# Optimization experiments

Measured on AMD Instinct MI355X. Metric: run time of the kernel, lower is better.

## Reference

```python
import jax, jax.numpy as jnp
import numpy as np

B, H, T, D = 4, 8, 1024, 64
DECAY = 0.95


def setup_inputs() -> dict:
    key = jax.random.key(0)
    kq, kk, kv = jax.random.split(key, 3)
    q = jax.random.normal(kq, (B, H, T, D), dtype=jnp.float32)
    k = jax.random.normal(kk, (B, H, T, D), dtype=jnp.float32)
    v = jax.random.normal(kv, (B, H, T, D), dtype=jnp.float32)
    return {"q": q, "k": k, "v": v}


def reference(q, k, v):
    """Recurrent KV (linear-attention) scan.

    State: S_t = decay * S_{t-1} + k_t outer v_t  (per batch/head, [D, D])
    Out:   o_t = q_t @ S_t                         ([D])
    """
    decay = jnp.float32(DECAY)

    def step(S, qkv_t):
        q_t, k_t, v_t = qkv_t  # each [B, H, D]
        S = decay * S + jnp.einsum('bhd,bhe->bhde', k_t, v_t)  # [B,H,D,D]
        o_t = jnp.einsum('bhd,bhde->bhe', q_t, S)              # [B,H,D]
        return S, o_t

    S0 = jnp.zeros((B, H, D, D), dtype=q.dtype)
    # time-major for scan: [T, B, H, D]
    qT = jnp.moveaxis(q, 2, 0)
    kT = jnp.moveaxis(k, 2, 0)
    vT = jnp.moveaxis(v, 2, 0)
    _, oT = jax.lax.scan(step, S0, (qT, kT, vT))
    return jnp.moveaxis(oT, 0, 2)  # [B, H, T, D]
```

## Files before the change

kernel.cpp:

```cpp
#include <hip/hip_runtime.h>
#include <hip/hip_bf16.h>

#define D_    64
#define BH    32
#define LCH   64
#define NC    16
#define DECAY 0.95f
#define LN_D  0.051293294f
#define DEC64 0.03752432f
#define LDSB  68

typedef __attribute__((ext_vector_type(8))) short          bf8_t;
typedef __attribute__((ext_vector_type(8))) unsigned short u16x8;
typedef __attribute__((ext_vector_type(4))) float          f32x4;
typedef unsigned short u16;

static __device__ __forceinline__ u16 f2bf(float f) {
    return __builtin_bit_cast(u16, __float2bfloat16(f));
}
static __device__ __forceinline__ bf8_t frag_rr(float4 a, float4 b, float sc) {
    u16x8 r;
    r[0] = f2bf(a.x * sc); r[1] = f2bf(a.y * sc); r[2] = f2bf(a.z * sc); r[3] = f2bf(a.w * sc);
    r[4] = f2bf(b.x * sc); r[5] = f2bf(b.y * sc); r[6] = f2bf(b.z * sc); r[7] = f2bf(b.w * sc);
    return __builtin_bit_cast(bf8_t, r);
}
static __device__ __forceinline__ bf8_t frag_g(const float* g) {
    u16x8 r;
    #pragma unroll
    for (int z = 0; z < 8; ++z) r[z] = f2bf(g[z]);
    return __builtin_bit_cast(bf8_t, r);
}

__global__ __launch_bounds__(256, 3) void kv_fused(const float* __restrict__ q,
                                                   const float* __restrict__ k,
                                                   const float* __restrict__ v,
                                                   float* __restrict__ o) {
    __shared__ u16 KT[2][D_][LDSB];
    __shared__ u16 VT[D_][LDSB];
    __shared__ u16 ST[D_][LDSB];
    __shared__ u16 As[LCH][LDSB];

    const int bid = (int)blockIdx.x;
    const int lb  = (bid & 7) * ((BH * NC) / 8) + (bid >> 3);
    const int bh  = lb >> 4;
    const int c   = lb & (NC - 1);

    const int tid  = threadIdx.x;
    const size_t bhb  = (size_t)bh * (NC * LCH) * D_;
    const size_t base = bhb + (size_t)c * LCH * D_;

    const int lane = tid & 63, w = tid >> 6;
    const int fr   = lane & 15, hi = lane >> 4;
    const int fk   = hi << 3;
    const int i0   = w << 4;
    const int ib   = i0 + (hi << 2);

    const int sj   = tid >> 2;
    const int sc0  = (tid & 3) << 4;
    const int sjx  = sj ^ ((tid & 3) << 4);

    float pv1[2][8], pv0[2][8];
    if (c >= 1) {
        const float* vs = v + base - (size_t)LCH * D_ + i0 + fr;
        #pragma unroll
        for (int kt = 0; kt < 2; ++kt)
            #pragma unroll
            for (int z = 0; z < 8; ++z)
                pv1[kt][z] = vs[(size_t)(kt * 32 + fk + z) * D_];
    }
    if (c >= 2) {
        const float* vs = v + base - (size_t)(2 * LCH) * D_ + i0 + fr;
        #pragma unroll
        for (int kt = 0; kt < 2; ++kt)
            #pragma unroll
            for (int z = 0; z < 8; ++z)
                pv0[kt][z] = vs[(size_t)(kt * 32 + fk + z) * D_];
    }
    const float* qrow = q + base + (size_t)(i0 + fr) * D_;
    const float4 qa0 = *(const float4*)(qrow + fk);
    const float4 qa1 = *(const float4*)(qrow + fk + 4);
    const float4 qb0 = *(const float4*)(qrow + 32 + fk);
    const float4 qb1 = *(const float4*)(qrow + 32 + fk + 4);
    float4 k1[4], k0[4];
    if (c >= 1) {
        const float* kg = k + base - (size_t)LCH * D_ + sj * D_ + sc0;
        #pragma unroll
        for (int m = 0; m < 4; ++m) k1[m] = *(const float4*)(kg + 4 * m);
    }
    if (c >= 2) {
        const float* kg = k + base - (size_t)(2 * LCH) * D_ + sj * D_ + sc0;
        #pragma unroll
        for (int m = 0; m < 4; ++m) k0[m] = *(const float4*)(kg + 4 * m);
    }
    float4 vo[4];
    {
        const float* vg = v + base + sj * D_ + sc0;
        #pragma unroll
        for (int m = 0; m < 4; ++m) vo[m] = *(const float4*)(vg + 4 * m);
    }

    const bf8_t aq0 = frag_rr(qa0, qa1, 1.f);
    const bf8_t aq1 = frag_rr(qb0, qb1, 1.f);
    bf8_t av1[2], av0[2];
    if (c >= 1) { av1[0] = frag_g(pv1[0]); av1[1] = frag_g(pv1[1]); }
    if (c >= 2) { av0[0] = frag_g(pv0[0]); av0[1] = frag_g(pv0[1]); }

    const float wdec = __expf(-LN_D * (float)(63 - sj));
    if (c >= 1) {
        #pragma unroll
        for (int m = 0; m < 4; ++m) {
            const int cb = sc0 + 4 * m;
            KT[1][cb + 0][sjx] = f2bf(k1[m].x * wdec);
            KT[1][cb + 1][sjx] = f2bf(k1[m].y * wdec);
            KT[1][cb + 2][sjx] = f2bf(k1[m].z * wdec);
            KT[1][cb + 3][sjx] = f2bf(k1[m].w * wdec);
        }
    }
    if (c >= 2) {
        const float wd0 = wdec * DEC64;
        #pragma unroll
        for (int m = 0; m < 4; ++m) {
            const int cb = sc0 + 4 * m;
            KT[0][cb + 0][sjx] = f2bf(k0[m].x * wd0);
            KT[0][cb + 1][sjx] = f2bf(k0[m].y * wd0);
            KT[0][cb + 2][sjx] = f2bf(k0[m].z * wd0);
            KT[0][cb + 3][sjx] = f2bf(k0[m].w * wd0);
        }
    }
    __syncthreads();

    float4 kp[4][4];
    #pragma unroll
    for (int jt = 0; jt < 4; ++jt) {
        if (jt <= w) {
            const float* krow = k + base + (size_t)(jt * 16 + fr) * D_;
            kp[jt][0] = *(const float4*)(krow + fk);
            kp[jt][1] = *(const float4*)(krow + fk + 4);
            kp[jt][2] = *(const float4*)(krow + 32 + fk);
            kp[jt][3] = *(const float4*)(krow + 32 + fk + 4);
        }
    }

    f32x4 accS[4];
    #pragma unroll
    for (int m = 0; m < 4; ++m) accS[m] = (f32x4){0.f, 0.f, 0.f, 0.f};
    __builtin_amdgcn_s_setprio(1);
    if (c >= 1) {
        #pragma unroll
        for (int kt = 0; kt < 2; ++kt)
            #pragma unroll
            for (int dt = 0; dt < 4; ++dt) {
                bf8_t bk = *(const bf8_t*)&KT[1][dt * 16 + fr][(kt * 32 + fk) ^ (dt << 4)];
                accS[dt] = __builtin_amdgcn_mfma_f32_16x16x32_bf16(av1[kt], bk, accS[dt], 0, 0, 0);
            }
    }
    if (c >= 2) {
        #pragma unroll
        for (int kt = 0; kt < 2; ++kt)
            #pragma unroll
            for (int dt = 0; dt < 4; ++dt) {
                bf8_t bk = *(const bf8_t*)&KT[0][dt * 16 + fr][(kt * 32 + fk) ^ (dt << 4)];
                accS[dt] = __builtin_amdgcn_mfma_f32_16x16x32_bf16(av0[kt], bk, accS[dt], 0, 0, 0);
            }
    }
    __builtin_amdgcn_s_setprio(0);

    if (c > 0) {
        #pragma unroll
        for (int dt = 0; dt < 4; ++dt)
            #pragma unroll
            for (int r = 0; r < 4; ++r)
                ST[ib + r][((dt ^ w) << 4) + fr] = f2bf(accS[dt][r]);
    }
    #pragma unroll
    for (int m = 0; m < 4; ++m) {
        const int cb = sc0 + 4 * m;
        VT[cb + 0][sjx] = f2bf(vo[m].x);
        VT[cb + 1][sjx] = f2bf(vo[m].y);
        VT[cb + 2][sjx] = f2bf(vo[m].z);
        VT[cb + 3][sjx] = f2bf(vo[m].w);
    }

    f32x4 accA[4];
    #pragma unroll
    for (int m = 0; m < 4; ++m) accA[m] = (f32x4){0.f, 0.f, 0.f, 0.f};
    __builtin_amdgcn_s_setprio(1);
    #pragma unroll
    for (int jt = 0; jt < 4; ++jt) {
        if (jt <= w) {
            const float ksc = __expf(LN_D * (float)(jt * 16 + fr));
            bf8_t b0 = frag_rr(kp[jt][0], kp[jt][1], ksc);
            bf8_t b1 = frag_rr(kp[jt][2], kp[jt][3], ksc);
            accA[jt] = __builtin_amdgcn_mfma_f32_16x16x32_bf16(aq0, b0, accA[jt], 0, 0, 0);
            accA[jt] = __builtin_amdgcn_mfma_f32_16x16x32_bf16(aq1, b1, accA[jt], 0, 0, 0);
        }
    }
    __builtin_amdgcn_s_setprio(0);

    const float db = __expf(-LN_D * (float)ib);
    float isc[4];
    isc[0] = db; isc[1] = db * DECAY; isc[2] = isc[1] * DECAY; isc[3] = isc[2] * DECAY;

    #pragma unroll
    for (int jt = 0; jt < 4; ++jt)
        #pragma unroll
        for (int r = 0; r < 4; ++r) {
            const int i  = ib + r;
            const int jj = jt * 16 + fr;
            float val = (jj <= i) ? accA[jt][r] * isc[r] : 0.f;
            As[i][jj] = f2bf(val);
        }
    __syncthreads();

    f32x4 accO[4];
    #pragma unroll
    for (int m = 0; m < 4; ++m) accO[m] = (f32x4){0.f, 0.f, 0.f, 0.f};
    __builtin_amdgcn_s_setprio(1);
    if (c > 0) {
        #pragma unroll
        for (int et = 0; et < 4; ++et) {
            bf8_t b0 = *(const bf8_t*)&ST[et * 16 + fr][(fk) ^ (et << 4)];
            bf8_t b1 = *(const bf8_t*)&ST[et * 16 + fr][(32 + fk) ^ (et << 4)];
            accO[et] = __builtin_amdgcn_mfma_f32_16x16x32_bf16(aq0, b0, accO[et], 0, 0, 0);
            accO[et] = __builtin_amdgcn_mfma_f32_16x16x32_bf16(aq1, b1, accO[et], 0, 0, 0);
        }
    }
    __builtin_amdgcn_s_setprio(0);
    #pragma unroll
    for (int et = 0; et < 4; ++et)
        #pragma unroll
        for (int r = 0; r < 4; ++r)
            accO[et][r] *= isc[r] * DECAY;

    const int nk2 = (w + 2) >> 1;
    __builtin_amdgcn_s_setprio(1);
    #pragma unroll
    for (int kt2 = 0; kt2 < 2; ++kt2) {
        if (kt2 < nk2) {
            bf8_t aa = *(const bf8_t*)&As[i0 + fr][kt2 * 32 + fk];
            #pragma unroll
            for (int et = 0; et < 4; ++et) {
                bf8_t bv = *(const bf8_t*)&VT[et * 16 + fr][(kt2 * 32 + fk) ^ (et << 4)];
                accO[et] = __builtin_amdgcn_mfma_f32_16x16x32_bf16(aa, bv, accO[et], 0, 0, 0);
            }
        }
    }
    __builtin_amdgcn_s_setprio(0);

    float* og = o + base;
    #pragma unroll
    for (int et = 0; et < 4; ++et)
        #pragma unroll
        for (int r = 0; r < 4; ++r)
            og[(size_t)(ib + r) * D_ + et * 16 + fr] = accO[et][r];
}

extern "C" void kernel_launch(void* const* d_in, const int* in_sizes, int n_in,
                              void* d_out, int out_size, void* d_ws, size_t ws_size,
                              hipStream_t stream) {
    const float* q = (const float*)d_in[0];
    const float* k = (const float*)d_in[1];
    const float* v = (const float*)d_in[2];
    kv_fused<<<BH * NC, 256, 0, stream>>>(q, k, v, (float*)d_out);
}
```

Before: 15.03 us.

## Split each chunk's work across 8 waves with 2-way column tiling

Doubles the block size from 256 to 512 threads and gives each row-tile wave pair a half of the output/state columns, so each wave does half the MFMAs and holds half the accumulators. Staging loads of K and V are redistributed over 8 lanes per row. This aims to raise per-block parallelism and hide latency for a small grid of 512 blocks, at the cost of duplicated q/v fragment loads per wave pair and more threads contending for the same LDS and barriers.

```diff
diff --git a/kernel.cpp b/kernel.cpp
--- a/kernel.cpp
+++ b/kernel.cpp
@@ -31,7 +31,7 @@
     return __builtin_bit_cast(bf8_t, r);
 }
 
-__global__ __launch_bounds__(256, 3) void kv_fused(const float* __restrict__ q,
+__global__ __launch_bounds__(512, 4) void kv_fused(const float* __restrict__ q,
                                                    const float* __restrict__ k,
                                                    const float* __restrict__ v,
                                                    float* __restrict__ o) {
@@ -49,15 +49,18 @@
     const size_t bhb  = (size_t)bh * (NC * LCH) * D_;
     const size_t base = bhb + (size_t)c * LCH * D_;
 
-    const int lane = tid & 63, w = tid >> 6;
+    const int lane = tid & 63;
+    const int w8   = tid >> 6;
+    const int wm   = w8 >> 1;
+    const int wn   = w8 & 1;
     const int fr   = lane & 15, hi = lane >> 4;
     const int fk   = hi << 3;
-    const int i0   = w << 4;
+    const int i0   = wm << 4;
     const int ib   = i0 + (hi << 2);
 
-    const int sj   = tid >> 2;
-    const int sc0  = (tid & 3) << 4;
-    const int sjx  = sj ^ ((tid & 3) << 4);
+    const int sj   = tid >> 3;
+    const int sc8  = (tid & 7) << 3;
+    const int sjx  = sj ^ (((sc8 >> 4) & 3) << 4);
 
     float pv1[2][8], pv0[2][8];
     if (c >= 1) {
@@ -81,22 +84,20 @@
     const float4 qa1 = *(const float4*)(qrow + fk + 4);
     const float4 qb0 = *(const float4*)(qrow + 32 + fk);
     const float4 qb1 = *(const float4*)(qrow + 32 + fk + 4);
-    float4 k1[4], k0[4];
-    if (c >= 1) {
-        const float* kg = k + base - (size_t)LCH * D_ + sj * D_ + sc0;
-        #pragma unroll
-        for (int m = 0; m < 4; ++m) k1[m] = *(const float4*)(kg + 4 * m);
-    }
-    if (c >= 2) {
-        const float* kg = k + base - (size_t)(2 * LCH) * D_ + sj * D_ + sc0;
-        #pragma unroll
-        for (int m = 0; m < 4; ++m) k0[m] = *(const float4*)(kg + 4 * m);
-    }
-    float4 vo[4];
+
+    float4 k1[2], k0[2];
+    if (c >= 1) {
+        const float* kg = k + base - (size_t)LCH * D_ + sj * D_ + sc8;
+        k1[0] = *(const float4*)kg;  k1[1] = *(const float4*)(kg + 4);
+    }
+    if (c >= 2) {
+        const float* kg = k + base - (size_t)(2 * LCH) * D_ + sj * D_ + sc8;
+        k0[0] = *(const float4*)kg;  k0[1] = *(const float4*)(kg + 4);
+    }
+    float4 vo[2];
     {
-        const float* vg = v + base + sj * D_ + sc0;
-        #pragma unroll
-        for (int m = 0; m < 4; ++m) vo[m] = *(const float4*)(vg + 4 * m);
+        const float* vg = v + base + sj * D_ + sc8;
+        vo[0] = *(const float4*)vg;  vo[1] = *(const float4*)(vg + 4);
     }
 
     const bf8_t aq0 = frag_rr(qa0, qa1, 1.f);
@@ -108,8 +109,8 @@
     const float wdec = __expf(-LN_D * (float)(63 - sj));
     if (c >= 1) {
         #pragma unroll
-        for (int m = 0; m < 4; ++m) {
-            const int cb = sc0 + 4 * m;
+        for (int m = 0; m < 2; ++m) {
+            const int cb = sc8 + 4 * m;
             KT[1][cb + 0][sjx] = f2bf(k1[m].x * wdec);
             KT[1][cb + 1][sjx] = f2bf(k1[m].y * wdec);
             KT[1][cb + 2][sjx] = f2bf(k1[m].z * wdec);
@@ -119,8 +120,8 @@
     if (c >= 2) {
         const float wd0 = wdec * DEC64;
         #pragma unroll
-        for (int m = 0; m < 4; ++m) {
-            const int cb = sc0 + 4 * m;
+        for (int m = 0; m < 2; ++m) {
+            const int cb = sc8 + 4 * m;
             KT[0][cb + 0][sjx] = f2bf(k0[m].x * wd0);
             KT[0][cb + 1][sjx] = f2bf(k0[m].y * wd0);
             KT[0][cb + 2][sjx] = f2bf(k0[m].z * wd0);
@@ -129,70 +130,74 @@
     }
     __syncthreads();
 
-    float4 kp[4][4];
-    #pragma unroll
-    for (int jt = 0; jt < 4; ++jt) {
-        if (jt <= w) {
+    float4 kp[2][4];
+    #pragma unroll
+    for (int jt2 = 0; jt2 < 2; ++jt2) {
+        const int jt = 2 * wn + jt2;
+        if (jt <= wm) {
             const float* krow = k + base + (size_t)(jt * 16 + fr) * D_;
-            kp[jt][0] = *(const float4*)(krow + fk);
-            kp[jt][1] = *(const float4*)(krow + fk + 4);
-            kp[jt][2] = *(const float4*)(krow + 32 + fk);
-            kp[jt][3] = *(const float4*)(krow + 32 + fk + 4);
-        }
-    }
-
-    f32x4 accS[4];
-    #pragma unroll
-    for (int m = 0; m < 4; ++m) accS[m] = (f32x4){0.f, 0.f, 0.f, 0.f};
-    __builtin_amdgcn_s_setprio(1);
-    if (c >= 1) {
-        #pragma unroll
-        for (int kt = 0; kt < 2; ++kt)
-            #pragma unroll
-            for (int dt = 0; dt < 4; ++dt) {
+            kp[jt2][0] = *(const float4*)(krow + fk);
+            kp[jt2][1] = *(const float4*)(krow + fk + 4);
+            kp[jt2][2] = *(const float4*)(krow + 32 + fk);
+            kp[jt2][3] = *(const float4*)(krow + 32 + fk + 4);
+        }
+    }
+
+    f32x4 accS[2];
+    accS[0] = (f32x4){0.f, 0.f, 0.f, 0.f};
+    accS[1] = (f32x4){0.f, 0.f, 0.f, 0.f};
+    __builtin_amdgcn_s_setprio(1);
+    if (c >= 1) {
+        #pragma unroll
+        for (int kt = 0; kt < 2; ++kt)
+            #pragma unroll
+            for (int dt2 = 0; dt2 < 2; ++dt2) {
+                const int dt = 2 * wn + dt2;
                 bf8_t bk = *(const bf8_t*)&KT[1][dt * 16 + fr][(kt * 32 + fk) ^ (dt << 4)];
-                accS[dt] = __builtin_amdgcn_mfma_f32_16x16x32_bf16(av1[kt], bk, accS[dt], 0, 0, 0);
-            }
-    }
-    if (c >= 2) {
-        #pragma unroll
-        for (int kt = 0; kt < 2; ++kt)
-            #pragma unroll
-            for (int dt = 0; dt < 4; ++dt) {
+                accS[dt2] = __builtin_amdgcn_mfma_f32_16x16x32_bf16(av1[kt], bk, accS[dt2], 0, 0, 0);
+            }
+    }
+    if (c >= 2) {
+        #pragma unroll
+        for (int kt = 0; kt < 2; ++kt)
+            #pragma unroll
+            for (int dt2 = 0; dt2 < 2; ++dt2) {
+                const int dt = 2 * wn + dt2;
                 bf8_t bk = *(const bf8_t*)&KT[0][dt * 16 + fr][(kt * 32 + fk) ^ (dt << 4)];
-                accS[dt] = __builtin_amdgcn_mfma_f32_16x16x32_bf16(av0[kt], bk, accS[dt], 0, 0, 0);
+                accS[dt2] = __builtin_amdgcn_mfma_f32_16x16x32_bf16(av0[kt], bk, accS[dt2], 0, 0, 0);
             }
     }
     __builtin_amdgcn_s_setprio(0);
 
     if (c > 0) {
         #pragma unroll
-        for (int dt = 0; dt < 4; ++dt)
+        for (int dt2 = 0; dt2 < 2; ++dt2)
             #pragma unroll
             for (int r = 0; r < 4; ++r)
-                ST[ib + r][((dt ^ w) << 4) + fr] = f2bf(accS[dt][r]);
-    }
-    #pragma unroll
-    for (int m = 0; m < 4; ++m) {
-        const int cb = sc0 + 4 * m;
+                ST[ib + r][(((2 * wn + dt2) ^ wm) << 4) + fr] = f2bf(accS[dt2][r]);
+    }
+    #pragma unroll
+    for (int m = 0; m < 2; ++m) {
+        const int cb = sc8 + 4 * m;
         VT[cb + 0][sjx] = f2bf(vo[m].x);
         VT[cb + 1][sjx] = f2bf(vo[m].y);
         VT[cb + 2][sjx] = f2bf(vo[m].z);
         VT[cb + 3][sjx] = f2bf(vo[m].w);
     }
 
-    f32x4 accA[4];
-    #pragma unroll
-    for (int m = 0; m < 4; ++m) accA[m] = (f32x4){0.f, 0.f, 0.f, 0.f};
-    __builtin_amdgcn_s_setprio(1);
-    #pragma unroll
-    for (int jt = 0; jt < 4; ++jt) {
-        if (jt <= w) {
+    f32x4 accA[2];
+    accA[0] = (f32x4){0.f, 0.f, 0.f, 0.f};
+    accA[1] = (f32x4){0.f, 0.f, 0.f, 0.f};
+    __builtin_amdgcn_s_setprio(1);
+    #pragma unroll
+    for (int jt2 = 0; jt2 < 2; ++jt2) {
+        const int jt = 2 * wn + jt2;
+        if (jt <= wm) {
             const float ksc = __expf(LN_D * (float)(jt * 16 + fr));
-            bf8_t b0 = frag_rr(kp[jt][0], kp[jt][1], ksc);
-            bf8_t b1 = frag_rr(kp[jt][2], kp[jt][3], ksc);
-            accA[jt] = __builtin_amdgcn_mfma_f32_16x16x32_bf16(aq0, b0, accA[jt], 0, 0, 0);
-            accA[jt] = __builtin_amdgcn_mfma_f32_16x16x32_bf16(aq1, b1, accA[jt], 0, 0, 0);
+            bf8_t b0 = frag_rr(kp[jt2][0], kp[jt2][1], ksc);
+            bf8_t b1 = frag_rr(kp[jt2][2], kp[jt2][3], ksc);
+            accA[jt2] = __builtin_amdgcn_mfma_f32_16x16x32_bf16(aq0, b0, accA[jt2], 0, 0, 0);
+            accA[jt2] = __builtin_amdgcn_mfma_f32_16x16x32_bf16(aq1, b1, accA[jt2], 0, 0, 0);
         }
     }
     __builtin_amdgcn_s_setprio(0);
@@ -202,46 +207,52 @@
     isc[0] = db; isc[1] = db * DECAY; isc[2] = isc[1] * DECAY; isc[3] = isc[2] * DECAY;
 
     #pragma unroll
-    for (int jt = 0; jt < 4; ++jt)
-        #pragma unroll
-        for (int r = 0; r < 4; ++r) {
-            const int i  = ib + r;
-            const int jj = jt * 16 + fr;
-            float val = (jj <= i) ? accA[jt][r] * isc[r] : 0.f;
-            As[i][jj] = f2bf(val);
-        }
+    for (int jt2 = 0; jt2 < 2; ++jt2) {
+        const int jt = 2 * wn + jt2;
+        if (jt <= wm + 1) {
+            #pragma unroll
+            for (int r = 0; r < 4; ++r) {
+                const int i  = ib + r;
+                const int jj = jt * 16 + fr;
+                float val = (jt <= wm && jj <= i) ? accA[jt2][r] * isc[r] : 0.f;
+                As[i][jj] = f2bf(val);
+            }
+        }
+    }
     __syncthreads();
 
-    f32x4 accO[4];
-    #pragma unroll
-    for (int m = 0; m < 4; ++m) accO[m] = (f32x4){0.f, 0.f, 0.f, 0.f};
+    f32x4 accO[2];
+    accO[0] = (f32x4){0.f, 0.f, 0.f, 0.f};
+    accO[1] = (f32x4){0.f, 0.f, 0.f, 0.f};
     __builtin_amdgcn_s_setprio(1);
     if (c > 0) {
         #pragma unroll
-        for (int et = 0; et < 4; ++et) {
+        for (int et2 = 0; et2 < 2; ++et2) {
+            const int et = 2 * wn + et2;
             bf8_t b0 = *(const bf8_t*)&ST[et * 16 + fr][(fk) ^ (et << 4)];
             bf8_t b1 = *(const bf8_t*)&ST[et * 16 + fr][(32 + fk) ^ (et << 4)];
-            accO[et] = __builtin_amdgcn_mfma_f32_16x16x32_bf16(aq0, b0, accO[et], 0, 0, 0);
-            accO[et] = __builtin_amdgcn_mfma_f32_16x16x32_bf16(aq1, b1, accO[et], 0, 0, 0);
-        }
-    }
-    __builtin_amdgcn_s_setprio(0);
-    #pragma unroll
-    for (int et = 0; et < 4; ++et)
+            accO[et2] = __builtin_amdgcn_mfma_f32_16x16x32_bf16(aq0, b0, accO[et2], 0, 0, 0);
+            accO[et2] = __builtin_amdgcn_mfma_f32_16x16x32_bf16(aq1, b1, accO[et2], 0, 0, 0);
+        }
+    }
+    __builtin_amdgcn_s_setprio(0);
+    #pragma unroll
+    for (int et2 = 0; et2 < 2; ++et2)
         #pragma unroll
         for (int r = 0; r < 4; ++r)
-            accO[et][r] *= isc[r] * DECAY;
-
-    const int nk2 = (w + 2) >> 1;
+            accO[et2][r] *= isc[r] * DECAY;
+
+    const int nk2 = (wm + 2) >> 1;
     __builtin_amdgcn_s_setprio(1);
     #pragma unroll
     for (int kt2 = 0; kt2 < 2; ++kt2) {
         if (kt2 < nk2) {
             bf8_t aa = *(const bf8_t*)&As[i0 + fr][kt2 * 32 + fk];
             #pragma unroll
-            for (int et = 0; et < 4; ++et) {
+            for (int et2 = 0; et2 < 2; ++et2) {
+                const int et = 2 * wn + et2;
                 bf8_t bv = *(const bf8_t*)&VT[et * 16 + fr][(kt2 * 32 + fk) ^ (et << 4)];
-                accO[et] = __builtin_amdgcn_mfma_f32_16x16x32_bf16(aa, bv, accO[et], 0, 0, 0);
+                accO[et2] = __builtin_amdgcn_mfma_f32_16x16x32_bf16(aa, bv, accO[et2], 0, 0, 0);
             }
         }
     }
@@ -249,10 +260,10 @@
 
     float* og = o + base;
     #pragma unroll
-    for (int et = 0; et < 4; ++et)
+    for (int et2 = 0; et2 < 2; ++et2)
         #pragma unroll
         for (int r = 0; r < 4; ++r)
-            og[(size_t)(ib + r) * D_ + et * 16 + fr] = accO[et][r];
+            og[(size_t)(ib + r) * D_ + (2 * wn + et2) * 16 + fr] = accO[et2][r];
 }
 
 extern "C" void kernel_launch(void* const* d_in, const int* in_sizes, int n_in,
@@ -261,5 +272,5 @@
     const float* q = (const float*)d_in[0];
     const float* k = (const float*)d_in[1];
     const float* v = (const float*)d_in[2];
-    kv_fused<<<BH * NC, 256, 0, stream>>>(q, k, v, (float*)d_out);
-}
+    kv_fused<<<BH * NC, 512, 0, stream>>>(q, k, v, (float*)d_out);
+}
```

Measured after the change: 14.42 us. 1.04x faster.
